# Kernel tuning notes

Measured on AMD Instinct MI355X. Metric: run time of the kernel, lower is better.

## Reference

```python
import jax, jax.numpy as jnp
import numpy as np

DEPTH, B, S, E, H, EXP = 6, 16, 511, 1024, 16, 2
HD = E // H
FF = EXP * E


def _layernorm(x, g, b, eps=1e-5):
    m = jnp.mean(x, axis=-1, keepdims=True)
    v = jnp.var(x, axis=-1, keepdims=True)
    return (x - m) * jax.lax.rsqrt(v + eps) * g + b


def setup_inputs() -> dict:
    key = jax.random.key(0)
    ks = jax.random.split(key, 12)
    sc = 0.02
    inp = {
        "x": jax.random.normal(ks[0], (B, S, E), jnp.float32),
        "cls_token": jax.random.normal(ks[1], (1, 1, E), jnp.float32),
        "pos_emb": jax.random.normal(ks[2], (1, S + 1, E), jnp.float32),
        # attention projections (bias=False in source), stacked over depth
        "Wq": jax.random.normal(ks[3], (DEPTH, E, E), jnp.float32) * sc,
        "Wk": jax.random.normal(ks[4], (DEPTH, E, E), jnp.float32) * sc,
        "Wv": jax.random.normal(ks[5], (DEPTH, E, E), jnp.float32) * sc,
        "Wp": jax.random.normal(ks[6], (DEPTH, E, E), jnp.float32) * sc,
        # layernorm params
        "ln1_g": jnp.ones((DEPTH, E), jnp.float32),
        "ln1_b": jnp.zeros((DEPTH, E), jnp.float32),
        "ln2_g": jnp.ones((DEPTH, E), jnp.float32),
        "ln2_b": jnp.zeros((DEPTH, E), jnp.float32),
        # feed-forward (with bias, as nn.Linear default)
        "W1": jax.random.normal(ks[7], (DEPTH, E, FF), jnp.float32) * sc,
        "b1": jnp.zeros((DEPTH, FF), jnp.float32),
        "W2": jax.random.normal(ks[8], (DEPTH, FF, E), jnp.float32) * sc,
        "b2": jnp.zeros((DEPTH, E), jnp.float32),
    }
    return inp


def reference(x, cls_token, pos_emb, Wq, Wk, Wv, Wp,
              ln1_g, ln1_b, ln2_g, ln2_b, W1, b1, W2, b2):
    b = x.shape[0]
    # AddClsToken + PositionalEmbedding
    h = jnp.concatenate([jnp.broadcast_to(cls_token, (b, 1, E)), x], axis=1) + pos_emb
    scale = jnp.asarray(E ** 0.5, h.dtype)  # source scales by sqrt(emb_size)
    for i in range(DEPTH):
        # --- self-attention sublayer (pre-LN) ---
        res = h
        xn = _layernorm(h, ln1_g[i], ln1_b[i])
        q = (xn @ Wq[i]).reshape(b, -1, H, HD).transpose(0, 2, 1, 3)  # b h n d
        k = (xn @ Wk[i]).reshape(b, -1, H, HD).transpose(0, 2, 1, 3)
        v = (xn @ Wv[i]).reshape(b, -1, H, HD).transpose(0, 2, 1, 3)
        energy = jnp.einsum('bhqd,bhkd->bhqk', q, k)
        att = jax.nn.softmax(energy / scale, axis=-1)
        out = jnp.einsum('bhqk,bhkd->bhqd', att, v)
        out = out.transpose(0, 2, 1, 3).reshape(b, -1, E)
        h = out @ Wp[i] + res
        # --- feed-forward sublayer (pre-LN) ---
        res = h
        yn = _layernorm(h, ln2_g[i], ln2_b[i])
        ff = jax.nn.gelu(yn @ W1[i] + b1[i], approximate=False) @ W2[i] + b2[i]
        h = ff + res
    return h
```

## Files before the change

### kernel.cpp

```cpp
#include <hip/hip_runtime.h>
#include <cstdint>
#include <cstddef>

#define DEPTH 6
#define NB    16
#define NSEQ  512
#define EMB   1024
#define NHEAD 16
#define HDIM  64
#define FFD   2048
#define NTOK  (NB * NSEQ)

typedef unsigned short u16;
using bf16x8 = __attribute__((ext_vector_type(8))) __bf16;
using f32x4  = __attribute__((ext_vector_type(4))) float;
using f32x16 = __attribute__((ext_vector_type(16))) float;
using u16x4  = __attribute__((ext_vector_type(4))) u16;
using u16x8  = __attribute__((ext_vector_type(8))) u16;

typedef __attribute__((address_space(1))) uint32_t* as1_u32p;
typedef __attribute__((address_space(3))) uint32_t* as3_u32p;

__device__ __forceinline__ u16 f2bf(float f) {
  union { float f; uint32_t u; } v; v.f = f;
  uint32_t u = v.u;
  return (u16)((u + 0x7FFFu + ((u >> 16) & 1u)) >> 16);
}

__device__ __forceinline__ void gload_lds16(const u16* g, u16* l) {
  void* gp = const_cast<u16*>(g);
  __builtin_amdgcn_global_load_lds((as1_u32p)gp, (as3_u32p)l, 16, 0, 0);
}

template<int ROWBYTES>
__device__ __forceinline__ void stage16k(const u16* g0, int ldk, u16* lds) {
  int t = threadIdx.x;
#pragma unroll
  for (int i = 0; i < 4; ++i) {
    int off = (i * 256 + t) * 16;
    int row = off / ROWBYTES;
    int pc  = (off % ROWBYTES) >> 4;
    int lc  = pc ^ (row & 7);
    gload_lds16(g0 + (size_t)row * ldk + lc * 8, lds + (off >> 1));
  }
}

__global__ __launch_bounds__(256)
void wprep_k(const float* __restrict__ W, u16* __restrict__ Wt,
             int K, int N, size_t inL, size_t outL, size_t outOff)
{
  int ntiles = N >> 6, ktiles = K >> 6;
  int bid = blockIdx.x;
  int l = bid / (ktiles * ntiles);
  int r = bid % (ktiles * ntiles);
  int kt = r / ntiles, nt = r % ntiles;
  const float* in = W + (size_t)l * inL + (size_t)(kt * 64) * N + nt * 64;
  u16* out = Wt + (size_t)l * outL + outOff + (size_t)(nt * 64) * K + kt * 64;
  __shared__ float tile[64][65];
  int t = threadIdx.x;
  int tr = t >> 4, tc = (t & 15) * 4;
#pragma unroll
  for (int i = 0; i < 4; ++i) {
    f32x4 v = *(const f32x4*)(in + (size_t)(tr + i * 16) * N + tc);
    tile[tr + i * 16][tc + 0] = v[0];
    tile[tr + i * 16][tc + 1] = v[1];
    tile[tr + i * 16][tc + 2] = v[2];
    tile[tr + i * 16][tc + 3] = v[3];
  }
  __syncthreads();
#pragma unroll
  for (int i = 0; i < 4; ++i) {
    int nr = tr + i * 16;
    u16x4 o;
    o[0] = f2bf(tile[tc + 0][nr]);
    o[1] = f2bf(tile[tc + 1][nr]);
    o[2] = f2bf(tile[tc + 2][nr]);
    o[3] = f2bf(tile[tc + 3][nr]);
    *(u16x4*)(out + (size_t)nr * K + tc) = o;
  }
}

__global__ __launch_bounds__(256)
void embed_k(const float* __restrict__ x, const float* __restrict__ cls,
             const float* __restrict__ pos, float* __restrict__ H)
{
  int row = blockIdx.x, t = threadIdx.x;
  int b_ = row >> 9, n = row & 511;
  int c = t * 4;
  f32x4 p = *(const f32x4*)(pos + (size_t)n * EMB + c);
  f32x4 s;
  if (n == 0) s = *(const f32x4*)(cls + c);
  else        s = *(const f32x4*)(x + ((size_t)b_ * 511 + (n - 1)) * EMB + c);
  f32x4 o = s + p;
  *(f32x4*)(H + (size_t)row * EMB + c) = o;
}

__global__ __launch_bounds__(256)
void ln_k(const float* __restrict__ H, const float* __restrict__ g,
          const float* __restrict__ b, u16* __restrict__ out)
{
  int lane = threadIdx.x & 63, w = threadIdx.x >> 6;
  int row = blockIdx.x * 4 + w;
  const float* hp = H + (size_t)row * EMB;
  f32x4 v[4];
  float s = 0.f, ss = 0.f;
#pragma unroll
  for (int i = 0; i < 4; ++i) {
    v[i] = *(const f32x4*)(hp + lane * 4 + i * 256);
#pragma unroll
    for (int j = 0; j < 4; ++j) { s += v[i][j]; ss += v[i][j] * v[i][j]; }
  }
#pragma unroll
  for (int m = 1; m <= 32; m <<= 1) { s += __shfl_xor(s, m); ss += __shfl_xor(ss, m); }
  float mean = s * (1.0f / EMB);
  float var  = ss * (1.0f / EMB) - mean * mean;
  float rs = rsqrtf(var + 1e-5f);
#pragma unroll
  for (int i = 0; i < 4; ++i) {
    f32x4 gg = *(const f32x4*)(g + lane * 4 + i * 256);
    f32x4 bb = *(const f32x4*)(b + lane * 4 + i * 256);
    u16x4 o;
#pragma unroll
    for (int j = 0; j < 4; ++j) o[j] = f2bf((v[i][j] - mean) * rs * gg[j] + bb[j]);
    *(u16x4*)(out + (size_t)row * EMB + lane * 4 + i * 256) = o;
  }
}

template<int EPI>
__global__ __launch_bounds__(256, 2)
void gemm_k(const u16* __restrict__ A, const u16* __restrict__ Bt,
            int nbn, int K,
            const float* __restrict__ bias, float* __restrict__ H,
            u16* __restrict__ outB,
            u16* __restrict__ qo, u16* __restrict__ ko, u16* __restrict__ vto)
{
  __shared__ u16 sm[2][16384];
  int cpx = gridDim.x >> 3;
  int logical = (blockIdx.x & 7) * cpx + (blockIdx.x >> 3);
  int bm = logical / nbn, bn = logical % nbn;
  int t = threadIdx.x, lane = t & 63, w = t >> 6;
  int wm = w >> 1, wn = w & 1;
  const u16* Ab = A  + (size_t)(bm * 128) * K;
  const u16* Bb = Bt + (size_t)(bn * 128) * K;
  int nkt = K >> 6;

  const f32x4 vzero = {0.f, 0.f, 0.f, 0.f};
  f32x4 acc[4][4];
#pragma unroll
  for (int i = 0; i < 4; ++i)
#pragma unroll
    for (int j = 0; j < 4; ++j) acc[i][j] = vzero;

  int r0 = lane & 15;
  int hi = lane >> 4;
  int kk0 = hi * 8;

  stage16k<128>(Ab, K, &sm[0][0]);
  stage16k<128>(Bb, K, &sm[0][8192]);
  stage16k<128>(Ab + 64, K, &sm[1][0]);
  stage16k<128>(Bb + 64, K, &sm[1][8192]);

  for (int kt = 0; kt < nkt; ++kt) {
    if (kt == nkt - 1) asm volatile("s_waitcnt vmcnt(0)" ::: "memory");
    else               asm volatile("s_waitcnt vmcnt(8)" ::: "memory");
    asm volatile("s_barrier" ::: "memory");
    const char* smAp = (const char*)&sm[kt & 1][0];
    const char* smBp = (const char*)&sm[kt & 1][8192];
#pragma unroll
    for (int ks = 0; ks < 2; ++ks) {
      int kk = ks * 32 + kk0;
      bf16x8 a[4], b[4];
#pragma unroll
      for (int mf = 0; mf < 4; ++mf) {
        int row = wm * 64 + mf * 16 + r0;
        a[mf] = *(const bf16x8*)(smAp + row * 128 + ((kk * 2) ^ ((row & 7) << 4)));
      }
#pragma unroll
      for (int nf = 0; nf < 4; ++nf) {
        int row = wn * 64 + nf * 16 + r0;
        b[nf] = *(const bf16x8*)(smBp + row * 128 + ((kk * 2) ^ ((row & 7) << 4)));
      }
#pragma unroll
      for (int mf = 0; mf < 4; ++mf)
#pragma unroll
        for (int nf = 0; nf < 4; ++nf)
          acc[mf][nf] = __builtin_amdgcn_mfma_f32_16x16x32_bf16(a[mf], b[nf], acc[mf][nf], 0, 0, 0);
    }
    asm volatile("s_barrier" ::: "memory");
    if (kt + 2 < nkt) {
      stage16k<128>(Ab + (kt + 2) * 64, K, &sm[kt & 1][0]);
      stage16k<128>(Bb + (kt + 2) * 64, K, &sm[kt & 1][8192]);
    }
  }

  if (EPI == 1 || EPI == 3) {
    int m0 = bm * 128 + wm * 64;
    int n0 = bn * 128 + wn * 64;
#pragma unroll
    for (int mf = 0; mf < 4; ++mf) {
#pragma unroll
      for (int nf = 0; nf < 4; ++nf) {
        int col  = n0 + nf * 16 + r0;
        int rowb = m0 + mf * 16 + hi * 4;
#pragma unroll
        for (int j = 0; j < 4; ++j) {
          float v = acc[mf][nf][j];
          size_t idx = (size_t)(rowb + j) * EMB + col;
          if (EPI == 1) H[idx] = v + H[idx];
          else          H[idx] = v + bias[col] + H[idx];
        }
      }
    }
    return;
  }

  u16* smE = &sm[0][0];
  int sec = (bn * 128) >> 10;
  bool vsec = (EPI == 0) && (sec == 2);
#pragma unroll
  for (int mf = 0; mf < 4; ++mf) {
#pragma unroll
    for (int nf = 0; nf < 4; ++nf) {
      int colL = wn * 64 + nf * 16 + r0;
#pragma unroll
      for (int j = 0; j < 4; ++j) {
        int rowL = wm * 64 + mf * 16 + hi * 4 + j;
        float v = acc[mf][nf][j];
        if (EPI == 2) {
          float xg = v + bias[bn * 128 + colL];
          v = 0.5f * xg * (1.0f + erff(xg * 0.70710678118654752f));
        }
        u16 o = f2bf(v);
        if (!vsec)
          smE[rowL * 128 + (colL & 7) + ((((colL >> 3) ^ (rowL & 7))) << 3)] = o;
        else
          smE[colL * 128 + (rowL & 7) + ((((rowL >> 3) ^ (colL & 7))) << 3)] = o;
      }
    }
  }
  __syncthreads();

  int c  = t & 15;
  int rb = t >> 4;
  if (!vsec) {
#pragma unroll
    for (int i = 0; i < 8; ++i) {
      int row = rb * 8 + i;
      u16x8 v = *(const u16x8*)(smE + row * 128 + ((c ^ (row & 7)) << 3));
      if (EPI == 2) {
        int rowg = bm * 128 + row;
        int colg = bn * 128 + c * 8;
        *(u16x8*)(outB + (size_t)rowg * FFD + colg) = v;
      } else {
        int n_ = bm * 128 + row;
        int b_ = n_ >> 9, tok = n_ & 511;
        int c0 = (bn * 128 - sec * 1024) + c * 8;
        int hh = c0 >> 6, d0 = c0 & 63;
        u16* dst = (sec == 0) ? qo : ko;
        *(u16x8*)(dst + (((size_t)(b_ * NHEAD + hh) * NSEQ + tok) * HDIM) + d0) = v;
      }
    }
  } else {
#pragma unroll
    for (int i = 0; i < 8; ++i) {
      int rowp = rb * 8 + i;
      u16x8 v = *(const u16x8*)(smE + rowp * 128 + ((c ^ (rowp & 7)) << 3));
      int c0 = (bn * 128 - 2048) + rowp;
      int hh = c0 >> 6, d = c0 & 63;
      int tok0 = bm * 128 + c * 8;
      int b_ = tok0 >> 9;
      *(u16x8*)(vto + ((size_t)(b_ * NHEAD + hh) * HDIM + d) * NSEQ + (tok0 & 511)) = v;
    }
  }
}

__global__ __launch_bounds__(256, 2)
void attn_k(const u16* __restrict__ Q, const u16* __restrict__ Kk,
            const u16* __restrict__ Vt, u16* __restrict__ AO)
{
  __shared__ u16 bufK[2][8192];
  __shared__ u16 bufV[2][8192];
  int bid = blockIdx.x;
  int logical = (bid & 7) * 128 + (bid >> 3);
  int bh = logical >> 2, qt = logical & 3;
  int t = threadIdx.x, lane = t & 63, w = t >> 6;
  int l31 = lane & 31, hi32 = lane >> 5;
  const u16* Kb = Kk + (size_t)bh * (NSEQ * HDIM);
  const u16* Vb = Vt + (size_t)bh * (HDIM * NSEQ);

  int qbase = qt * 128 + w * 32;
  const u16* Qp = Q + ((size_t)bh * NSEQ + qbase + l31) * HDIM;
  bf16x8 qf[4];
#pragma unroll
  for (int tk = 0; tk < 4; ++tk)
    qf[tk] = *(const bf16x8*)(Qp + 16 * tk + 8 * hi32);

  stage16k<128>(Kb, HDIM, &bufK[0][0]);
  stage16k<256>(Vb, NSEQ, &bufV[0][0]);
  __syncthreads();

  f32x16 accO[2];
#pragma unroll
  for (int r = 0; r < 16; ++r) { accO[0][r] = 0.f; accO[1][r] = 0.f; }
  float m_run = -1e30f, den = 0.f;
  const float inv32 = 0.03125f;

  for (int c = 0; c < 4; ++c) {
    if (c < 3) {
      stage16k<128>(Kb + (size_t)(c + 1) * 128 * HDIM, HDIM, &bufK[(c + 1) & 1][0]);
      stage16k<256>(Vb + (c + 1) * 128, NSEQ, &bufV[(c + 1) & 1][0]);
    }
    const char* smK = (const char*)&bufK[c & 1][0];
    f32x16 s[4];
#pragma unroll
    for (int kt = 0; kt < 4; ++kt) {
#pragma unroll
      for (int r = 0; r < 16; ++r) s[kt][r] = 0.f;
#pragma unroll
      for (int tk = 0; tk < 4; ++tk) {
        int row = kt * 32 + l31;
        bf16x8 kf = *(const bf16x8*)(smK + row * 128 +
                      ((32 * tk + 16 * hi32) ^ ((row & 7) << 4)));
        s[kt] = __builtin_amdgcn_mfma_f32_32x32x16_bf16(kf, qf[tk], s[kt], 0, 0, 0);
      }
    }
    float mc = -1e30f;
#pragma unroll
    for (int kt = 0; kt < 4; ++kt)
#pragma unroll
      for (int r = 0; r < 16; ++r) mc = fmaxf(mc, s[kt][r]);
    mc = fmaxf(mc, __shfl_xor(mc, 32));
    float newm = fmaxf(m_run, mc);
    float fac = __expf((m_run - newm) * inv32);
    den *= fac;
#pragma unroll
    for (int r = 0; r < 16; ++r) { accO[0][r] *= fac; accO[1][r] *= fac; }
    m_run = newm;
#pragma unroll
    for (int kt = 0; kt < 4; ++kt)
#pragma unroll
      for (int r = 0; r < 16; ++r) {
        float p = __expf((s[kt][r] - newm) * inv32);
        den += p;
        s[kt][r] = p;
      }
    uint32_t pb[32];
#pragma unroll
    for (int j = 0; j < 32; ++j) {
      float lo = s[j >> 3][(2 * j) & 15];
      float hi = s[j >> 3][((2 * j) & 15) + 1];
      asm("v_cvt_pk_bf16_f32 %0, %1, %2" : "=v"(pb[j]) : "v"(lo), "v"(hi));
    }
    const char* smV = (const char*)&bufV[c & 1][0];
#pragma unroll
    for (int ks = 0; ks < 8; ++ks) {
      uint32_t x0 = pb[4 * ks], y0 = pb[4 * ks + 2];
      uint32_t x1 = pb[4 * ks + 1], y1 = pb[4 * ks + 3];
      asm("v_permlane32_swap_b32 %0, %1" : "+v"(x0), "+v"(y0));
      asm("v_permlane32_swap_b32 %0, %1" : "+v"(x1), "+v"(y1));
      union { uint4 u; bf16x8 v; } pa;
      pa.u = make_uint4(x0, x1, y0, y1);
#pragma unroll
      for (int dt = 0; dt < 2; ++dt) {
        int row = dt * 32 + l31;
        bf16x8 vb = *(const bf16x8*)(smV + row * 256 +
                      ((32 * ks + 16 * hi32) ^ ((row & 7) << 4)));
        accO[dt] = __builtin_amdgcn_mfma_f32_32x32x16_bf16(pa.v, vb, accO[dt], 0, 0, 0);
      }
    }
    __syncthreads();
  }

  float denf = den + __shfl_xor(den, 32);
  float rden = 1.0f / denf;
  int b_ = bh >> 4, hh = bh & 15;
#pragma unroll
  for (int r = 0; r < 16; ++r) {
    int qoff = (r & 3) + 8 * (r >> 2) + 4 * hi32;
    float rd = __shfl(rden, qoff);
    int tok = qbase + qoff;
    size_t base = ((size_t)(b_ * NSEQ + tok)) * EMB + hh * 64 + l31;
    AO[base]      = f2bf(accO[0][r] * rd);
    AO[base + 32] = f2bf(accO[1][r] * rd);
  }
}

extern "C" void kernel_launch(void* const* d_in, const int* in_sizes, int n_in,
                              void* d_out, int out_size, void* d_ws, size_t ws_size,
                              hipStream_t stream)
{
  const float* x    = (const float*)d_in[0];
  const float* cls  = (const float*)d_in[1];
  const float* pos  = (const float*)d_in[2];
  const float* Wq   = (const float*)d_in[3];
  const float* Wk   = (const float*)d_in[4];
  const float* Wv   = (const float*)d_in[5];
  const float* Wp   = (const float*)d_in[6];
  const float* ln1g = (const float*)d_in[7];
  const float* ln1b = (const float*)d_in[8];
  const float* ln2g = (const float*)d_in[9];
  const float* ln2b = (const float*)d_in[10];
  const float* W1   = (const float*)d_in[11];
  const float* b1   = (const float*)d_in[12];
  const float* W2   = (const float*)d_in[13];
  const float* b2   = (const float*)d_in[14];
  float* H = (float*)d_out;

  char* ws = (char*)d_ws;
  u16* wqkv = (u16*)(ws + 0);
  u16* wp   = (u16*)(ws + 37748736);
  u16* w1t  = (u16*)(ws + 50331648);
  u16* w2t  = (u16*)(ws + 75497472);
  u16* xn   = (u16*)(ws + 100663296);
  u16* qb   = (u16*)(ws + 117440512);
  u16* kb   = (u16*)(ws + 134217728);
  u16* vtb  = (u16*)(ws + 150994944);
  u16* ffb  = qb;

  wprep_k<<<1536, 256, 0, stream>>>(Wq, wqkv, 1024, 1024, 1048576, 3145728, 0);
  wprep_k<<<1536, 256, 0, stream>>>(Wk, wqkv, 1024, 1024, 1048576, 3145728, 1048576);
  wprep_k<<<1536, 256, 0, stream>>>(Wv, wqkv, 1024, 1024, 1048576, 3145728, 2097152);
  wprep_k<<<1536, 256, 0, stream>>>(Wp, wp,   1024, 1024, 1048576, 1048576, 0);
  wprep_k<<<3072, 256, 0, stream>>>(W1, w1t,  1024, 2048, 2097152, 2097152, 0);
  wprep_k<<<3072, 256, 0, stream>>>(W2, w2t,  2048, 1024, 2097152, 2097152, 0);

  embed_k<<<NTOK, 256, 0, stream>>>(x, cls, pos, H);

  for (int l = 0; l < DEPTH; ++l) {
    ln_k<<<2048, 256, 0, stream>>>(H, ln1g + l * EMB, ln1b + l * EMB, xn);
    gemm_k<0><<<64 * 24, 256, 0, stream>>>(xn, wqkv + (size_t)l * 3145728, 24, 1024,
                                           nullptr, nullptr, nullptr, qb, kb, vtb);
    attn_k<<<1024, 256, 0, stream>>>(qb, kb, vtb, xn);
    gemm_k<1><<<64 * 8, 256, 0, stream>>>(xn, wp + (size_t)l * 1048576, 8, 1024,
                                          nullptr, H, nullptr, nullptr, nullptr, nullptr);
    ln_k<<<2048, 256, 0, stream>>>(H, ln2g + l * EMB, ln2b + l * EMB, xn);
    gemm_k<2><<<64 * 16, 256, 0, stream>>>(xn, w1t + (size_t)l * 2097152, 16, 1024,
                                           b1 + l * FFD, nullptr, ffb, nullptr, nullptr, nullptr);
    gemm_k<3><<<64 * 8, 256, 0, stream>>>(ffb, w2t + (size_t)l * 2097152, 8, 2048,
                                          b2 + l * EMB, H, nullptr, nullptr, nullptr, nullptr);
  }
}
```

Measured before the change: 1.461 ms.

## Single-buffer GEMM for occupancy, pipeline attention K/V, merge weight prep

The GEMM kernel drops its double-buffered LDS prefetch in favour of a single 32KB buffer with synchronous stage-then-sync, and raises launch bounds to 3 blocks per CU to hide latency through occupancy instead. The attention kernel switches to a two-ahead prefetch of K/V chunks with explicit vmcnt waits and raises wave priority around its MFMA blocks. The six weight-prep launches are merged into one kernel. The risk is that the GEMM loses load/compute overlap, and the higher occupancy may not make up for it.

```diff
diff --git a/kernel.cpp b/kernel.cpp
--- a/kernel.cpp
+++ b/kernel.cpp
@@ -46,16 +46,35 @@
 }
 
 __global__ __launch_bounds__(256)
-void wprep_k(const float* __restrict__ W, u16* __restrict__ Wt,
-             int K, int N, size_t inL, size_t outL, size_t outOff)
-{
+void wprep_all(const float* __restrict__ Wq, const float* __restrict__ Wk,
+               const float* __restrict__ Wv, const float* __restrict__ Wp,
+               const float* __restrict__ W1, const float* __restrict__ W2,
+               u16* __restrict__ wqkv, u16* __restrict__ wp,
+               u16* __restrict__ w1t, u16* __restrict__ w2t)
+{
+  int bid = blockIdx.x;
+  const float* W; u16* out; int K, N; size_t inL, outL, outOff; int r;
+  if (bid < 4608) {
+    int which = bid / 1536; r = bid % 1536;
+    W = (which == 0) ? Wq : (which == 1) ? Wk : Wv;
+    out = wqkv; K = 1024; N = 1024;
+    inL = 1048576; outL = 3145728; outOff = (size_t)which * 1048576;
+  } else if (bid < 6144) {
+    W = Wp; out = wp; r = bid - 4608; K = 1024; N = 1024;
+    inL = 1048576; outL = 1048576; outOff = 0;
+  } else if (bid < 9216) {
+    W = W1; out = w1t; r = bid - 6144; K = 1024; N = 2048;
+    inL = 2097152; outL = 2097152; outOff = 0;
+  } else {
+    W = W2; out = w2t; r = bid - 9216; K = 2048; N = 1024;
+    inL = 2097152; outL = 2097152; outOff = 0;
+  }
   int ntiles = N >> 6, ktiles = K >> 6;
-  int bid = blockIdx.x;
-  int l = bid / (ktiles * ntiles);
-  int r = bid % (ktiles * ntiles);
-  int kt = r / ntiles, nt = r % ntiles;
+  int l = r / (ktiles * ntiles);
+  int rr = r % (ktiles * ntiles);
+  int kt = rr / ntiles, nt = rr % ntiles;
   const float* in = W + (size_t)l * inL + (size_t)(kt * 64) * N + nt * 64;
-  u16* out = Wt + (size_t)l * outL + outOff + (size_t)(nt * 64) * K + kt * 64;
+  u16* o = out + (size_t)l * outL + outOff + (size_t)(nt * 64) * K + kt * 64;
   __shared__ float tile[64][65];
   int t = threadIdx.x;
   int tr = t >> 4, tc = (t & 15) * 4;
@@ -71,12 +90,12 @@
 #pragma unroll
   for (int i = 0; i < 4; ++i) {
     int nr = tr + i * 16;
-    u16x4 o;
-    o[0] = f2bf(tile[tc + 0][nr]);
-    o[1] = f2bf(tile[tc + 1][nr]);
-    o[2] = f2bf(tile[tc + 2][nr]);
-    o[3] = f2bf(tile[tc + 3][nr]);
-    *(u16x4*)(out + (size_t)nr * K + tc) = o;
+    u16x4 ov;
+    ov[0] = f2bf(tile[tc + 0][nr]);
+    ov[1] = f2bf(tile[tc + 1][nr]);
+    ov[2] = f2bf(tile[tc + 2][nr]);
+    ov[3] = f2bf(tile[tc + 3][nr]);
+    *(u16x4*)(o + (size_t)nr * K + tc) = ov;
   }
 }
 
@@ -127,14 +146,14 @@
 }
 
 template<int EPI>
-__global__ __launch_bounds__(256, 2)
+__global__ __launch_bounds__(256, 3)
 void gemm_k(const u16* __restrict__ A, const u16* __restrict__ Bt,
             int nbn, int K,
             const float* __restrict__ bias, float* __restrict__ H,
             u16* __restrict__ outB,
             u16* __restrict__ qo, u16* __restrict__ ko, u16* __restrict__ vto)
 {
-  __shared__ u16 sm[2][16384];
+  __shared__ u16 sm[16384];
   int cpx = gridDim.x >> 3;
   int logical = (blockIdx.x & 7) * cpx + (blockIdx.x >> 3);
   int bm = logical / nbn, bn = logical % nbn;
@@ -155,17 +174,12 @@
   int hi = lane >> 4;
   int kk0 = hi * 8;
 
-  stage16k<128>(Ab, K, &sm[0][0]);
-  stage16k<128>(Bb, K, &sm[0][8192]);
-  stage16k<128>(Ab + 64, K, &sm[1][0]);
-  stage16k<128>(Bb + 64, K, &sm[1][8192]);
-
   for (int kt = 0; kt < nkt; ++kt) {
-    if (kt == nkt - 1) asm volatile("s_waitcnt vmcnt(0)" ::: "memory");
-    else               asm volatile("s_waitcnt vmcnt(8)" ::: "memory");
-    asm volatile("s_barrier" ::: "memory");
-    const char* smAp = (const char*)&sm[kt & 1][0];
-    const char* smBp = (const char*)&sm[kt & 1][8192];
+    stage16k<128>(Ab + kt * 64, K, sm);
+    stage16k<128>(Bb + kt * 64, K, sm + 8192);
+    __syncthreads();
+    const char* smAp = (const char*)sm;
+    const char* smBp = (const char*)(sm + 8192);
 #pragma unroll
     for (int ks = 0; ks < 2; ++ks) {
       int kk = ks * 32 + kk0;
@@ -186,11 +200,7 @@
         for (int nf = 0; nf < 4; ++nf)
           acc[mf][nf] = __builtin_amdgcn_mfma_f32_16x16x32_bf16(a[mf], b[nf], acc[mf][nf], 0, 0, 0);
     }
-    asm volatile("s_barrier" ::: "memory");
-    if (kt + 2 < nkt) {
-      stage16k<128>(Ab + (kt + 2) * 64, K, &sm[kt & 1][0]);
-      stage16k<128>(Bb + (kt + 2) * 64, K, &sm[kt & 1][8192]);
-    }
+    __syncthreads();
   }
 
   if (EPI == 1 || EPI == 3) {
@@ -214,7 +224,6 @@
     return;
   }
 
-  u16* smE = &sm[0][0];
   int sec = (bn * 128) >> 10;
   bool vsec = (EPI == 0) && (sec == 2);
 #pragma unroll
@@ -232,9 +241,9 @@
         }
         u16 o = f2bf(v);
         if (!vsec)
-          smE[rowL * 128 + (colL & 7) + ((((colL >> 3) ^ (rowL & 7))) << 3)] = o;
+          sm[rowL * 128 + (colL & 7) + ((((colL >> 3) ^ (rowL & 7))) << 3)] = o;
         else
-          smE[colL * 128 + (rowL & 7) + ((((rowL >> 3) ^ (colL & 7))) << 3)] = o;
+          sm[colL * 128 + (rowL & 7) + ((((rowL >> 3) ^ (colL & 7))) << 3)] = o;
       }
     }
   }
@@ -246,7 +255,7 @@
 #pragma unroll
     for (int i = 0; i < 8; ++i) {
       int row = rb * 8 + i;
-      u16x8 v = *(const u16x8*)(smE + row * 128 + ((c ^ (row & 7)) << 3));
+      u16x8 v = *(const u16x8*)(sm + row * 128 + ((c ^ (row & 7)) << 3));
       if (EPI == 2) {
         int rowg = bm * 128 + row;
         int colg = bn * 128 + c * 8;
@@ -264,7 +273,7 @@
 #pragma unroll
     for (int i = 0; i < 8; ++i) {
       int rowp = rb * 8 + i;
-      u16x8 v = *(const u16x8*)(smE + rowp * 128 + ((c ^ (rowp & 7)) << 3));
+      u16x8 v = *(const u16x8*)(sm + rowp * 128 + ((c ^ (rowp & 7)) << 3));
       int c0 = (bn * 128 - 2048) + rowp;
       int hh = c0 >> 6, d = c0 & 63;
       int tok0 = bm * 128 + c * 8;
@@ -297,7 +306,8 @@
 
   stage16k<128>(Kb, HDIM, &bufK[0][0]);
   stage16k<256>(Vb, NSEQ, &bufV[0][0]);
-  __syncthreads();
+  stage16k<128>(Kb + 128 * HDIM, HDIM, &bufK[1][0]);
+  stage16k<256>(Vb + 128, NSEQ, &bufV[1][0]);
 
   f32x16 accO[2];
 #pragma unroll
@@ -306,12 +316,12 @@
   const float inv32 = 0.03125f;
 
   for (int c = 0; c < 4; ++c) {
-    if (c < 3) {
-      stage16k<128>(Kb + (size_t)(c + 1) * 128 * HDIM, HDIM, &bufK[(c + 1) & 1][0]);
-      stage16k<256>(Vb + (c + 1) * 128, NSEQ, &bufV[(c + 1) & 1][0]);
-    }
+    if (c == 3) asm volatile("s_waitcnt vmcnt(0)" ::: "memory");
+    else        asm volatile("s_waitcnt vmcnt(8)" ::: "memory");
+    asm volatile("s_barrier" ::: "memory");
     const char* smK = (const char*)&bufK[c & 1][0];
     f32x16 s[4];
+    __builtin_amdgcn_s_setprio(1);
 #pragma unroll
     for (int kt = 0; kt < 4; ++kt) {
 #pragma unroll
@@ -324,6 +334,7 @@
         s[kt] = __builtin_amdgcn_mfma_f32_32x32x16_bf16(kf, qf[tk], s[kt], 0, 0, 0);
       }
     }
+    __builtin_amdgcn_s_setprio(0);
     float mc = -1e30f;
 #pragma unroll
     for (int kt = 0; kt < 4; ++kt)
@@ -360,6 +371,7 @@
       asm("v_permlane32_swap_b32 %0, %1" : "+v"(x1), "+v"(y1));
       union { uint4 u; bf16x8 v; } pa;
       pa.u = make_uint4(x0, x1, y0, y1);
+      __builtin_amdgcn_s_setprio(1);
 #pragma unroll
       for (int dt = 0; dt < 2; ++dt) {
         int row = dt * 32 + l31;
@@ -367,8 +379,13 @@
                       ((32 * ks + 16 * hi32) ^ ((row & 7) << 4)));
         accO[dt] = __builtin_amdgcn_mfma_f32_32x32x16_bf16(pa.v, vb, accO[dt], 0, 0, 0);
       }
-    }
-    __syncthreads();
+      __builtin_amdgcn_s_setprio(0);
+    }
+    asm volatile("s_barrier" ::: "memory");
+    if (c + 2 < 4) {
+      stage16k<128>(Kb + (size_t)(c + 2) * 128 * HDIM, HDIM, &bufK[c & 1][0]);
+      stage16k<256>(Vb + (c + 2) * 128, NSEQ, &bufV[c & 1][0]);
+    }
   }
 
   float denf = den + __shfl_xor(den, 32);
@@ -417,13 +434,8 @@
   u16* vtb  = (u16*)(ws + 150994944);
   u16* ffb  = qb;
 
-  wprep_k<<<1536, 256, 0, stream>>>(Wq, wqkv, 1024, 1024, 1048576, 3145728, 0);
-  wprep_k<<<1536, 256, 0, stream>>>(Wk, wqkv, 1024, 1024, 1048576, 3145728, 1048576);
-  wprep_k<<<1536, 256, 0, stream>>>(Wv, wqkv, 1024, 1024, 1048576, 3145728, 2097152);
-  wprep_k<<<1536, 256, 0, stream>>>(Wp, wp,   1024, 1024, 1048576, 1048576, 0);
-  wprep_k<<<3072, 256, 0, stream>>>(W1, w1t,  1024, 2048, 2097152, 2097152, 0);
-  wprep_k<<<3072, 256, 0, stream>>>(W2, w2t,  2048, 1024, 2097152, 2097152, 0);
-
+  wprep_all<<<12288, 256, 0, stream>>>(Wq, Wk, Wv, Wp, W1, W2,
+                                       wqkv, wp, w1t, w2t);
   embed_k<<<NTOK, 256, 0, stream>>>(x, cls, pos, H);
 
   for (int l = 0; l < DEPTH; ++l) {
```

After: 1.410 ms. 1.04x faster.
